# Kernel optimization log

Measured on AMD Instinct MI355X. Metric: run time of the kernel, lower is better.

The kernel has to match this reference:

```python
import jax, jax.numpy as jnp
import numpy as np

B, N, E = 64, 256, 512   # batch, leaves (power of 2), embed_size
D, U = 512, 512          # tree_size, units (controller size == units)


def setup_inputs() -> dict:
    key = jax.random.key(0)
    ks = jax.random.split(key, 11)
    sc = lambda k, shape: jax.random.normal(k, shape, dtype=jnp.float32) * 0.05
    return {
        "inputs": jax.random.normal(ks[0], (B, N, E), dtype=jnp.float32),
        "h0": sc(ks[1], (B, U)),
        "c0": sc(ks[2], (B, U)),
        "W_t": sc(ks[3], (E, D)),          # Transformer
        "W_j": sc(ks[4], (2 * D, D)),      # Join
        "W_s": sc(ks[5], (D + U, 1)),      # Search
        "W_h": sc(ks[6], (D + U, D)),      # Write candidate
        "W_T": sc(ks[7], (D + U, 1)),      # Write gate
        "kernel": sc(ks[8], (E, 4 * U)),   # LSTM input kernel (i,f,c,o)
        "rec_kernel": sc(ks[9], (U, 4 * U)),
        "bias": jnp.zeros((4 * U,), jnp.float32),
    }


def reference(inputs, h0, c0, W_t, W_j, W_s, W_h, W_T, kernel, rec_kernel, bias):
    b, n, e = inputs.shape
    control = h0  # control = previous LSTM hidden state

    # --- leaf embed: Transformer, batched over all leaves ---
    leaf_h = jax.nn.relu(jnp.einsum('bne,ed->bnd', inputs, W_t))  # [B,N,D]

    # --- refresh: bottom-up join, batched per tree level ---
    levels = [leaf_h]
    h = leaf_h
    while h.shape[1] > 1:
        pair = jnp.concatenate([h[:, 0::2], h[:, 1::2]], axis=-1)  # [B,m/2,2D]
        h = jax.nn.relu(jnp.einsum('bmk,kd->bmd', pair, W_j))
        levels.append(h)

    # --- retrieve: top-down search producing leaf attentions ---
    # Searches all use refresh-time h (parent search happens before any
    # update in its subtree), so a level-batched top-down pass is exact.
    attn = jnp.ones((b, 1, 1), inputs.dtype)
    for lvl in range(len(levels) - 1, 0, -1):
        node_h = levels[lvl]                     # [B,m,D]
        m = node_h.shape[1]
        ctrl = jnp.broadcast_to(control[:, None, :], (b, m, control.shape[-1]))
        mr = jax.nn.sigmoid(jnp.einsum('bmk,ko->bmo',
                                       jnp.concatenate([node_h, ctrl], -1), W_s))  # [B,m,1]
        # children interleave: left gets attn*(1-mr), right gets attn*mr
        attn = jnp.concatenate([attn * (1.0 - mr), attn * mr], axis=-1).reshape(b, 2 * m, 1)

    tree_out = jnp.sum(attn * inputs, axis=1)  # [B,E] soft-retrieved leaf value

    # --- write update of leaf memories, batched over all leaves ---
    ctrl = jnp.broadcast_to(control[:, None, :], (b, n, control.shape[-1]))
    data = jnp.concatenate([leaf_h, ctrl], -1)                     # [B,N,D+U]
    cand = jax.nn.sigmoid(jnp.einsum('bnk,kd->bnd', data, W_h))
    upd = jax.nn.sigmoid(jnp.einsum('bnk,ko->bno', data, W_T))
    written = upd * cand + (1.0 - upd) * leaf_h
    leaf_h_new = attn * written + (1.0 - attn) * leaf_h            # [B,N,D]

    # --- LSTM cell update (keras LSTMCell gate order i,f,c,o) ---
    z = tree_out @ kernel + h0 @ rec_kernel + bias
    zi, zf, zg, zo = jnp.split(z, 4, axis=-1)
    c_new = jax.nn.sigmoid(zf) * c0 + jax.nn.sigmoid(zi) * jnp.tanh(zg)
    h_new = jax.nn.sigmoid(zo) * jnp.tanh(c_new)
    return h_new, c_new, leaf_h_new
```

## Files before the change

### kernel.cpp

```cpp
#include <hip/hip_runtime.h>
#include <hip/hip_bf16.h>
#include <cstdint>
#include <cstddef>


__device__ __forceinline__ float sigmoidf_(float x) { return 1.0f / (1.0f + __expf(-x)); }

typedef __attribute__((ext_vector_type(8))) short bf16x8;
typedef __attribute__((ext_vector_type(4))) float f32x4;

__device__ __forceinline__ void load_lds16(const void* g, void* l) {
  __builtin_amdgcn_global_load_lds((const __attribute__((address_space(1))) void*)g,
                                   (__attribute__((address_space(3))) void*)l, 16, 0, 0);
}

__global__ __launch_bounds__(256)
void cvt_inputs(const float* __restrict__ in, __hip_bfloat16* __restrict__ outp) {
  const size_t i = ((size_t)blockIdx.x * 256 + threadIdx.x) * 8;
  float4 v0 = *(const float4*)(in + i);
  float4 v1 = *(const float4*)(in + i + 4);
  union { __hip_bfloat16 h[8]; bf16x8 v; } u;
  u.h[0] = __float2bfloat16(v0.x); u.h[1] = __float2bfloat16(v0.y);
  u.h[2] = __float2bfloat16(v0.z); u.h[3] = __float2bfloat16(v0.w);
  u.h[4] = __float2bfloat16(v1.x); u.h[5] = __float2bfloat16(v1.y);
  u.h[6] = __float2bfloat16(v1.z); u.h[7] = __float2bfloat16(v1.w);
  *(bf16x8*)(outp + i) = u.v;
}

__global__ __launch_bounds__(256)
void tconv_all(const float* __restrict__ W_t, const float* __restrict__ W_j,
               const float* __restrict__ W_h,
               __hip_bfloat16* __restrict__ Wt_t, __hip_bfloat16* __restrict__ Wt_j,
               __hip_bfloat16* __restrict__ Wt_h) {
  const int z = blockIdx.z;
  if (z != 1 && blockIdx.x >= 16) return;
  const int K = (z == 1) ? 1024 : 512;
  const float* W = (z == 0) ? W_t : ((z == 1) ? W_j : W_h);
  __hip_bfloat16* Wt = (z == 0) ? Wt_t : ((z == 1) ? Wt_j : Wt_h);
  __shared__ float sh[32][33];
  const int tx = threadIdx.x & 31, ty = threadIdx.x >> 5;
  const int k0 = blockIdx.x * 32, n0 = blockIdx.y * 32;
#pragma unroll
  for (int i = 0; i < 4; ++i)
    sh[ty + i * 8][tx] = W[(size_t)(k0 + ty + i * 8) * 512 + n0 + tx];
  __syncthreads();
#pragma unroll
  for (int i = 0; i < 4; ++i)
    Wt[(size_t)(n0 + ty + i * 8) * K + k0 + tx] = __float2bfloat16(sh[tx][ty + i * 8]);
}

template<int MODE, bool AFP32>
__global__ __launch_bounds__(256)
void mfma_gemm(const __hip_bfloat16* __restrict__ A, const float* __restrict__ Af,
               const __hip_bfloat16* __restrict__ Bt, int M, int K,
               __hip_bfloat16* __restrict__ Cb, float* __restrict__ Cf,
               const float* __restrict__ ctrl_h, const float* __restrict__ attn,
               const float* __restrict__ upd, const __hip_bfloat16* __restrict__ leaf) {
  __shared__ __align__(16) __hip_bfloat16 Asm[2][128 * 32];
  __shared__ __align__(16) __hip_bfloat16 Bsm[2][128 * 32];
  const int tid = threadIdx.x;
  const int wave = tid >> 6, lane = tid & 63;
  const int bm = blockIdx.x * 128, bn = blockIdx.y * 128;
  const int wm = (wave >> 1) * 64, wn = (wave & 1) * 64;
  const int q = lane >> 4, lr = lane & 15;

  f32x4 acc[4][4] = {};

  const int c0 = wave * 128 + lane, c1 = c0 + 64;
  const size_t ga0 = (size_t)(bm + (c0 >> 2)) * K + (c0 & 3) * 8;
  const size_t ga1 = (size_t)(bm + (c1 >> 2)) * K + (c1 & 3) * 8;
  const size_t gb0 = (size_t)(bn + (c0 >> 2)) * K + (c0 & 3) * 8;
  const size_t gb1 = (size_t)(bn + (c1 >> 2)) * K + (c1 & 3) * 8;

  if constexpr (AFP32) {
    for (int k0v = 0; k0v < K; k0v += 32) {
#pragma unroll
      for (int it = 0; it < 4; ++it) {
        const int c = it * 256 + tid;
        const int row = c >> 3, kc = c & 7;
        float4 v = *(const float4*)(Af + (size_t)(bm + row) * K + k0v + kc * 4);
        __hip_bfloat16 h[4] = {__float2bfloat16(v.x), __float2bfloat16(v.y),
                               __float2bfloat16(v.z), __float2bfloat16(v.w)};
        *(ushort4*)(Asm[0] + row * 32 + kc * 4) = *(ushort4*)h;
      }
      load_lds16(Bt + gb0 + k0v, Bsm[0] + wave * 1024);
      load_lds16(Bt + gb1 + k0v, Bsm[0] + wave * 1024 + 512);
      __syncthreads();
      bf16x8 af[4], bfr[4];
#pragma unroll
      for (int mt = 0; mt < 4; ++mt)
        af[mt] = *(const bf16x8*)(Asm[0] + (wm + mt * 16 + lr) * 32 + q * 8);
#pragma unroll
      for (int nt = 0; nt < 4; ++nt)
        bfr[nt] = *(const bf16x8*)(Bsm[0] + (wn + nt * 16 + lr) * 32 + q * 8);
#pragma unroll
      for (int mt = 0; mt < 4; ++mt)
#pragma unroll
        for (int nt = 0; nt < 4; ++nt)
          acc[mt][nt] = __builtin_amdgcn_mfma_f32_16x16x32_bf16(af[mt], bfr[nt], acc[mt][nt], 0, 0, 0);
      __syncthreads();
    }
  } else {
    auto stage = [&](int s, int kv) {
      load_lds16(A + ga0 + kv, Asm[s] + wave * 1024);
      load_lds16(A + ga1 + kv, Asm[s] + wave * 1024 + 512);
      load_lds16(Bt + gb0 + kv, Bsm[s] + wave * 1024);
      load_lds16(Bt + gb1 + kv, Bsm[s] + wave * 1024 + 512);
    };
    stage(0, 0);
    __syncthreads();
    int cur = 0;
    for (int kv = 0; kv < K; kv += 32) {
      if (kv + 32 < K) stage(cur ^ 1, kv + 32);
      bf16x8 af[4], bfr[4];
#pragma unroll
      for (int mt = 0; mt < 4; ++mt)
        af[mt] = *(const bf16x8*)(Asm[cur] + (wm + mt * 16 + lr) * 32 + q * 8);
#pragma unroll
      for (int nt = 0; nt < 4; ++nt)
        bfr[nt] = *(const bf16x8*)(Bsm[cur] + (wn + nt * 16 + lr) * 32 + q * 8);
#pragma unroll
      for (int mt = 0; mt < 4; ++mt)
#pragma unroll
        for (int nt = 0; nt < 4; ++nt)
          acc[mt][nt] = __builtin_amdgcn_mfma_f32_16x16x32_bf16(af[mt], bfr[nt], acc[mt][nt], 0, 0, 0);
      __syncthreads();
      cur ^= 1;
    }
  }

  if (MODE == 0) {
#pragma unroll
    for (int mt = 0; mt < 4; ++mt) {
      const int rbase = bm + wm + mt * 16 + q * 4;
#pragma unroll
      for (int nt = 0; nt < 4; ++nt) {
        const int col = bn + wn + nt * 16 + lr;
#pragma unroll
        for (int r = 0; r < 4; ++r) {
          const int row = rbase + r;
          if (row < M)
            Cb[(size_t)row * 512 + col] = __float2bfloat16(fmaxf(acc[mt][nt][r], 0.f));
        }
      }
    }
  } else {
#pragma unroll
    for (int mt = 0; mt < 4; ++mt) {
      const int rbase = bm + wm + mt * 16 + q * 4;
#pragma unroll
      for (int r = 0; r < 4; ++r) {
        const int row = rbase + r;
        const float a = attn[row];
        const float u = upd[row];
        const int bidx = row >> 8;
#pragma unroll
        for (int nt = 0; nt < 4; ++nt) {
          const int col = bn + wn + nt * 16 + lr;
          const float cand = sigmoidf_(acc[mt][nt][r] + ctrl_h[(size_t)bidx * 512 + col]);
          const float lf = __bfloat162float(leaf[(size_t)row * 512 + col]);
          const float w = u * cand + (1.f - u) * lf;
          Cf[(size_t)row * 512 + col] = a * w + (1.f - a) * lf;
        }
      }
    }
  }
}

__global__ __launch_bounds__(256)
void join_level(const __hip_bfloat16* __restrict__ in, __hip_bfloat16* __restrict__ outp,
                const __hip_bfloat16* __restrict__ Wt_j) {
  const int wave = threadIdx.x >> 6, lane = threadIdx.x & 63;
  const int q = lane >> 4, lr = lane & 15;
  const int tile = blockIdx.x * 4 + wave;
  const int mtile = tile >> 5, ntile = tile & 31;
  const __hip_bfloat16* ap = in + (size_t)(mtile * 16 + lr) * 1024 + q * 8;
  const __hip_bfloat16* bp = Wt_j + (size_t)(ntile * 16 + lr) * 1024 + q * 8;
  f32x4 acc = {0.f, 0.f, 0.f, 0.f};
#pragma unroll 8
  for (int k0 = 0; k0 < 1024; k0 += 32) {
    bf16x8 a  = *(const bf16x8*)(ap + k0);
    bf16x8 bb = *(const bf16x8*)(bp + k0);
    acc = __builtin_amdgcn_mfma_f32_16x16x32_bf16(a, bb, acc, 0, 0, 0);
  }
  const int col = ntile * 16 + lr;
  const int orow = mtile * 16 + q * 4;
#pragma unroll
  for (int r = 0; r < 4; ++r)
    outp[(size_t)(orow + r) * 512 + col] = __float2bfloat16(fmaxf(acc[r], 0.f));
}

__global__ __launch_bounds__(256)
void gemv_upd(const __hip_bfloat16* __restrict__ leaf, const float* __restrict__ W_T,
              const float* __restrict__ ctrlT, float* __restrict__ upd) {
  const int wave = threadIdx.x >> 6, lane = threadIdx.x & 63;
  const int row = blockIdx.x * 4 + wave;
  union { bf16x8 v; __hip_bfloat16 e[8]; } u;
  u.v = *(const bf16x8*)(leaf + (size_t)row * 512 + lane * 8);
  const float* wp = W_T + lane * 8;
  float p = 0.f;
#pragma unroll
  for (int j = 0; j < 8; ++j) p += __bfloat162float(u.e[j]) * wp[j];
#pragma unroll
  for (int off = 32; off > 0; off >>= 1) p += __shfl_down(p, off);
  if (lane == 0) upd[row] = sigmoidf_(p + ctrlT[row >> 8]);
}

__global__ __launch_bounds__(256)
void ctrl_prep(const float* __restrict__ h0, const float* __restrict__ W_h,
               const float* __restrict__ W_T, float* __restrict__ ch,
               float* __restrict__ ctrlT) {
  const int b = blockIdx.y, tid = threadIdx.x;
  if (blockIdx.x == 2) {
    __shared__ float part[256];
    float p = 0.f;
    for (int i = tid; i < 512; i += 256) p += h0[b * 512 + i] * W_T[512 + i];
    part[tid] = p; __syncthreads();
    for (int s = 128; s > 0; s >>= 1) { if (tid < s) part[tid] += part[tid + s]; __syncthreads(); }
    if (tid == 0) ctrlT[b] = part[0];
  } else {
    __shared__ float hsh[512];
    hsh[tid]       = h0[b * 512 + tid];
    hsh[tid + 256] = h0[b * 512 + 256 + tid];
    __syncthreads();
    const int col = blockIdx.x * 256 + tid;
    const float* Wp = W_h + (size_t)512 * 512 + col;
    float s = 0.f;
#pragma unroll 8
    for (int k = 0; k < 512; ++k) s += hsh[k] * Wp[(size_t)k * 512];
    ch[(size_t)b * 512 + col] = s;
  }
}

__global__ __launch_bounds__(256)
void propagate_sc(const __hip_bfloat16* __restrict__ levels, const float* __restrict__ h0,
                  const float* __restrict__ W_s, float* __restrict__ attn_out) {
  const int b = blockIdx.x, tid = threadIdx.x;
  const int wave = tid >> 6, lane = tid & 63;
  __shared__ float part[256], ws[512], sc_sh[256], attn_sh[256], newattn[256];
  __shared__ float scs_sh;
  ws[tid] = W_s[tid]; ws[tid + 256] = W_s[tid + 256];
  float p = 0.f;
  for (int i = tid; i < 512; i += 256) p += h0[b * 512 + i] * W_s[512 + i];
  part[tid] = p; __syncthreads();
  for (int s = 128; s > 0; s >>= 1) { if (tid < s) part[tid] += part[tid + s]; __syncthreads(); }
  if (tid == 0) { scs_sh = part[0]; attn_sh[0] = 1.f; }
  __syncthreads();
  const float scs = scs_sh;
  const int rowbase[9] = {0, 0, 8192, 12288, 14336, 15360, 15872, 16128, 16256};
  const int nodeoff[9] = {0, 0, 128, 192, 224, 240, 248, 252, 254};
  for (int l = 1; l <= 8; ++l) {
    const int m = 256 >> l;
    for (int j0 = wave * 8; j0 < m; j0 += 32) {
      const int j = j0 + (lane >> 3), s = lane & 7;
      float q = 0.f;
      if (j < m) {
        const __hip_bfloat16* xr = levels + (size_t)(rowbase[l] + b * m + j) * 512;
#pragma unroll
        for (int i = 0; i < 8; ++i) {
          const int k = (i * 8 + s) * 8;
          union { bf16x8 v; __hip_bfloat16 e[8]; } u;
          u.v = *(const bf16x8*)(xr + k);
#pragma unroll
          for (int jj = 0; jj < 8; ++jj) q += __bfloat162float(u.e[jj]) * ws[k + jj];
        }
      }
      q += __shfl_xor(q, 1); q += __shfl_xor(q, 2); q += __shfl_xor(q, 4);
      if (s == 0 && j < m) sc_sh[nodeoff[l] + j] = q;
    }
  }
  __syncthreads();
#pragma unroll
  for (int l = 8; l >= 1; --l) {
    const int m = 256 >> l;
    if (tid < m) {
      const float mr = sigmoidf_(sc_sh[nodeoff[l] + tid] + scs);
      const float a = attn_sh[tid];
      newattn[2 * tid]     = a * (1.f - mr);
      newattn[2 * tid + 1] = a * mr;
    }
    __syncthreads();
    if (tid < 2 * m) attn_sh[tid] = newattn[tid];
    __syncthreads();
  }
  attn_out[b * 256 + tid] = attn_sh[tid];
}

__global__ __launch_bounds__(256)
void tree_part(const float* __restrict__ inputs, const float* __restrict__ attn,
               float* __restrict__ tp) {
  const int s = blockIdx.x, b = blockIdx.y;
  const int tid = threadIdx.x;
  __shared__ float a_sh[64];
  if (tid < 64) a_sh[tid] = attn[b * 256 + s * 64 + tid];
  __syncthreads();
  float acc0 = 0.f, acc1 = 0.f;
  const float* base = inputs + ((size_t)b * 256 + s * 64) * 512;
  for (int nn = 0; nn < 64; ++nn) {
    const float a = a_sh[nn];
    const float* row = base + (size_t)nn * 512;
    acc0 += a * row[tid];
    acc1 += a * row[tid + 256];
  }
  tp[((size_t)s * 64 + b) * 512 + tid]       = acc0;
  tp[((size_t)s * 64 + b) * 512 + tid + 256] = acc1;
}

__global__ __launch_bounds__(256)
void lstm_fused(const float* __restrict__ tp, const float* __restrict__ h0,
                const float* __restrict__ kern, const float* __restrict__ rec,
                const float* __restrict__ bias, const float* __restrict__ c0,
                float* __restrict__ out_h, float* __restrict__ out_c) {
  const int tid = threadIdx.x;
  const int ug = tid & 63, gate = tid >> 6;
  const int b0 = blockIdx.y * 4;
  __shared__ float xs[4][512], hs[4][512];
  for (int i = tid; i < 2048; i += 256) {
    const int bb = i >> 9, k = i & 511;
    const size_t idx = (size_t)(b0 + bb) * 512 + k;
    xs[bb][k] = tp[idx] + tp[32768 + idx] + tp[65536 + idx] + tp[98304 + idx];
    hs[bb][k] = h0[idx];
  }
  __syncthreads();
  const int col = gate * 512 + blockIdx.x * 64 + ug;
  float a0 = bias[col], a1 = a0, a2 = a0, a3 = a0;
#pragma unroll 4
  for (int k = 0; k < 512; ++k) {
    const float wk = kern[(size_t)k * 2048 + col];
    const float wr = rec[(size_t)k * 2048 + col];
    a0 += xs[0][k] * wk + hs[0][k] * wr;
    a1 += xs[1][k] * wk + hs[1][k] * wr;
    a2 += xs[2][k] * wk + hs[2][k] * wr;
    a3 += xs[3][k] * wk + hs[3][k] * wr;
  }
  __shared__ float zs[4][4][64];
  zs[gate][0][ug] = a0; zs[gate][1][ug] = a1;
  zs[gate][2][ug] = a2; zs[gate][3][ug] = a3;
  __syncthreads();
  const int cb = tid >> 6, cu = tid & 63;
  const float zi = zs[0][cb][cu], zf = zs[1][cb][cu];
  const float zg = zs[2][cb][cu], zo = zs[3][cb][cu];
  const int gi = (b0 + cb) * 512 + blockIdx.x * 64 + cu;
  const float c = sigmoidf_(zf) * c0[gi] + sigmoidf_(zi) * tanhf(zg);
  out_h[gi] = sigmoidf_(zo) * tanhf(c);
  out_c[gi] = c;
}

extern "C" void kernel_launch(void* const* d_in, const int* in_sizes, int n_in,
                              void* d_out, int out_size, void* d_ws, size_t ws_size,
                              hipStream_t stream) {
  const float* inputs = (const float*)d_in[0];
  const float* h0     = (const float*)d_in[1];
  const float* c0     = (const float*)d_in[2];
  const float* W_t    = (const float*)d_in[3];
  const float* W_j    = (const float*)d_in[4];
  const float* W_s    = (const float*)d_in[5];
  const float* W_h    = (const float*)d_in[6];
  const float* W_T    = (const float*)d_in[7];
  const float* kern   = (const float*)d_in[8];
  const float* rec    = (const float*)d_in[9];
  const float* bias   = (const float*)d_in[10];
  float* out = (float*)d_out;

  char* p = (char*)d_ws;
  __hip_bfloat16* leaf_bf   = (__hip_bfloat16*)p; p += 16777216;
  __hip_bfloat16* levels_bf = (__hip_bfloat16*)p; p += 16842752;
  __hip_bfloat16* Wt_t      = (__hip_bfloat16*)p; p += 524288;
  __hip_bfloat16* Wt_j      = (__hip_bfloat16*)p; p += 1048576;
  __hip_bfloat16* Wt_h      = (__hip_bfloat16*)p; p += 524288;
  float* attn  = (float*)p; p += 65536;
  float* upd   = (float*)p; p += 65536;
  float* ch    = (float*)p; p += 131072;
  float* ctrlT = (float*)p; p += 4096;
  float* tp    = (float*)p; p += 524288;
  const bool use_cvt = ws_size >= (size_t)(p - (char*)d_ws) + 16777216;
  __hip_bfloat16* inputs_bf = (__hip_bfloat16*)p;

  tconv_all<<<dim3(32, 16, 3), 256, 0, stream>>>(W_t, W_j, W_h, Wt_t, Wt_j, Wt_h);
  ctrl_prep<<<dim3(3, 64), 256, 0, stream>>>(h0, W_h, W_T, ch, ctrlT);

  if (use_cvt) {
    cvt_inputs<<<4096, 256, 0, stream>>>(inputs, inputs_bf);
    mfma_gemm<0, false><<<dim3(128, 4), 256, 0, stream>>>(
        inputs_bf, nullptr, Wt_t, 16384, 512,
        leaf_bf, nullptr, nullptr, nullptr, nullptr, nullptr);
  } else {
    mfma_gemm<0, true><<<dim3(128, 4), 256, 0, stream>>>(
        nullptr, inputs, Wt_t, 16384, 512,
        leaf_bf, nullptr, nullptr, nullptr, nullptr, nullptr);
  }

  const int lvl_off_h[9] = {0, 0, 4194304, 6291456, 7340032,
                            7864320, 8126464, 8257536, 8323072};
  const __hip_bfloat16* Aptr = leaf_bf;
  for (int l = 1; l <= 3; ++l) {
    const int M = 64 * (256 >> l);
    __hip_bfloat16* Cl = levels_bf + lvl_off_h[l];
    mfma_gemm<0, false><<<dim3(M / 128, 4), 256, 0, stream>>>(
        Aptr, nullptr, Wt_j, M, 1024,
        Cl, nullptr, nullptr, nullptr, nullptr, nullptr);
    Aptr = Cl;
  }
  for (int l = 4; l <= 8; ++l) {
    const int m_out = 256 >> l;
    join_level<<<32 * m_out, 256, 0, stream>>>(levels_bf + lvl_off_h[l - 1],
                                               levels_bf + lvl_off_h[l], Wt_j);
  }

  gemv_upd<<<4096, 256, 0, stream>>>(leaf_bf, W_T, ctrlT, upd);
  propagate_sc<<<64, 256, 0, stream>>>(levels_bf, h0, W_s, attn);

  tree_part<<<dim3(4, 64), 256, 0, stream>>>(inputs, attn, tp);

  mfma_gemm<1, false><<<dim3(128, 4), 256, 0, stream>>>(
      leaf_bf, nullptr, Wt_h, 16384, 512,
      nullptr, out + 65536, ch, attn, upd, leaf_bf);

  lstm_fused<<<dim3(8, 16), 256, 0, stream>>>(tp, h0, kern, rec, bias, c0, out, out + 32768);
}
```

Measured before the change: 389.7 us.

## Fuse upd gemv into leaf GEMM epilogue and split-K the LSTM gate GEMM

```diff
diff --git a/kernel.cpp b/kernel.cpp
--- a/kernel.cpp
+++ b/kernel.cpp
@@ -55,7 +55,8 @@
                const __hip_bfloat16* __restrict__ Bt, int M, int K,
                __hip_bfloat16* __restrict__ Cb, float* __restrict__ Cf,
                const float* __restrict__ ctrl_h, const float* __restrict__ attn,
-               const float* __restrict__ upd, const __hip_bfloat16* __restrict__ leaf) {
+               const float* __restrict__ upd_raw, const __hip_bfloat16* __restrict__ leaf,
+               const float* __restrict__ W_T, const float* __restrict__ ctrlT) {
   __shared__ __align__(16) __hip_bfloat16 Asm[2][128 * 32];
   __shared__ __align__(16) __hip_bfloat16 Bsm[2][128 * 32];
   const int tid = threadIdx.x;
@@ -144,6 +145,27 @@
         }
       }
     }
+    if (upd_raw) {
+      float wt[4];
+#pragma unroll
+      for (int nt = 0; nt < 4; ++nt) wt[nt] = W_T[bn + wn + nt * 16 + lr];
+#pragma unroll
+      for (int mt = 0; mt < 4; ++mt) {
+        const int rbase = bm + wm + mt * 16 + q * 4;
+#pragma unroll
+        for (int r = 0; r < 4; ++r) {
+          float p = 0.f;
+#pragma unroll
+          for (int nt = 0; nt < 4; ++nt) {
+            const float v = __bfloat162float(__float2bfloat16(fmaxf(acc[mt][nt][r], 0.f)));
+            p += v * wt[nt];
+          }
+          p += __shfl_xor(p, 1); p += __shfl_xor(p, 2);
+          p += __shfl_xor(p, 4); p += __shfl_xor(p, 8);
+          if (lr == 0) atomicAdd((float*)&upd_raw[rbase + r], p);
+        }
+      }
+    }
   } else {
 #pragma unroll
     for (int mt = 0; mt < 4; ++mt) {
@@ -152,8 +174,8 @@
       for (int r = 0; r < 4; ++r) {
         const int row = rbase + r;
         const float a = attn[row];
-        const float u = upd[row];
         const int bidx = row >> 8;
+        const float u = sigmoidf_(upd_raw[row] + ctrlT[bidx]);
 #pragma unroll
         for (int nt = 0; nt < 4; ++nt) {
           const int col = bn + wn + nt * 16 + lr;
@@ -188,22 +210,6 @@
 #pragma unroll
   for (int r = 0; r < 4; ++r)
     outp[(size_t)(orow + r) * 512 + col] = __float2bfloat16(fmaxf(acc[r], 0.f));
-}
-
-__global__ __launch_bounds__(256)
-void gemv_upd(const __hip_bfloat16* __restrict__ leaf, const float* __restrict__ W_T,
-              const float* __restrict__ ctrlT, float* __restrict__ upd) {
-  const int wave = threadIdx.x >> 6, lane = threadIdx.x & 63;
-  const int row = blockIdx.x * 4 + wave;
-  union { bf16x8 v; __hip_bfloat16 e[8]; } u;
-  u.v = *(const bf16x8*)(leaf + (size_t)row * 512 + lane * 8);
-  const float* wp = W_T + lane * 8;
-  float p = 0.f;
-#pragma unroll
-  for (int j = 0; j < 8; ++j) p += __bfloat162float(u.e[j]) * wp[j];
-#pragma unroll
-  for (int off = 32; off > 0; off >>= 1) p += __shfl_down(p, off);
-  if (lane == 0) upd[row] = sigmoidf_(p + ctrlT[row >> 8]);
 }
 
 __global__ __launch_bounds__(256)
@@ -307,43 +313,59 @@
 }
 
 __global__ __launch_bounds__(256)
-void lstm_fused(const float* __restrict__ tp, const float* __restrict__ h0,
-                const float* __restrict__ kern, const float* __restrict__ rec,
-                const float* __restrict__ bias, const float* __restrict__ c0,
-                float* __restrict__ out_h, float* __restrict__ out_c) {
+void lstm_gemm_splitk(const float* __restrict__ tp, const float* __restrict__ h0,
+                      const float* __restrict__ kern, const float* __restrict__ rec,
+                      float* __restrict__ Zp) {
   const int tid = threadIdx.x;
-  const int ug = tid & 63, gate = tid >> 6;
+  const int col = blockIdx.x * 256 + tid;
   const int b0 = blockIdx.y * 4;
-  __shared__ float xs[4][512], hs[4][512];
-  for (int i = tid; i < 2048; i += 256) {
-    const int bb = i >> 9, k = i & 511;
-    const size_t idx = (size_t)(b0 + bb) * 512 + k;
-    xs[bb][k] = tp[idx] + tp[32768 + idx] + tp[65536 + idx] + tp[98304 + idx];
-    hs[bb][k] = h0[idx];
+  const int z = blockIdx.z;
+  const float* W = (z < 4) ? (kern + (size_t)z * 128 * 2048)
+                           : (rec + (size_t)(z - 4) * 128 * 2048);
+  const int koff = (z & 3) * 128;
+  __shared__ float xs[4][128];
+  for (int i = tid; i < 512; i += 256) {
+    int bb = i >> 7, k = i & 127;
+    const size_t idx = (size_t)(b0 + bb) * 512 + koff + k;
+    float x;
+    if (z < 4) x = tp[idx] + tp[32768 + idx] + tp[65536 + idx] + tp[98304 + idx];
+    else       x = h0[idx];
+    xs[bb][k] = x;
   }
   __syncthreads();
-  const int col = gate * 512 + blockIdx.x * 64 + ug;
-  float a0 = bias[col], a1 = a0, a2 = a0, a3 = a0;
-#pragma unroll 4
-  for (int k = 0; k < 512; ++k) {
-    const float wk = kern[(size_t)k * 2048 + col];
-    const float wr = rec[(size_t)k * 2048 + col];
-    a0 += xs[0][k] * wk + hs[0][k] * wr;
-    a1 += xs[1][k] * wk + hs[1][k] * wr;
-    a2 += xs[2][k] * wk + hs[2][k] * wr;
-    a3 += xs[3][k] * wk + hs[3][k] * wr;
-  }
-  __shared__ float zs[4][4][64];
-  zs[gate][0][ug] = a0; zs[gate][1][ug] = a1;
-  zs[gate][2][ug] = a2; zs[gate][3][ug] = a3;
-  __syncthreads();
-  const int cb = tid >> 6, cu = tid & 63;
-  const float zi = zs[0][cb][cu], zf = zs[1][cb][cu];
-  const float zg = zs[2][cb][cu], zo = zs[3][cb][cu];
-  const int gi = (b0 + cb) * 512 + blockIdx.x * 64 + cu;
-  const float c = sigmoidf_(zf) * c0[gi] + sigmoidf_(zi) * tanhf(zg);
-  out_h[gi] = sigmoidf_(zo) * tanhf(c);
-  out_c[gi] = c;
+  float a0 = 0.f, a1 = 0.f, a2 = 0.f, a3 = 0.f;
+#pragma unroll 8
+  for (int k = 0; k < 128; ++k) {
+    const float w = W[(size_t)k * 2048 + col];
+    a0 += xs[0][k] * w;
+    a1 += xs[1][k] * w;
+    a2 += xs[2][k] * w;
+    a3 += xs[3][k] * w;
+  }
+  Zp[((size_t)z * 64 + b0 + 0) * 2048 + col] = a0;
+  Zp[((size_t)z * 64 + b0 + 1) * 2048 + col] = a1;
+  Zp[((size_t)z * 64 + b0 + 2) * 2048 + col] = a2;
+  Zp[((size_t)z * 64 + b0 + 3) * 2048 + col] = a3;
+}
+
+__global__ __launch_bounds__(256)
+void lstm_combine(const float* __restrict__ Zp, const float* __restrict__ bias,
+                  const float* __restrict__ c0,
+                  float* __restrict__ out_h, float* __restrict__ out_c) {
+  const int i = blockIdx.x * 256 + threadIdx.x;
+  const int b = i >> 9, u = i & 511;
+  float zi = bias[u], zf = bias[512 + u], zg = bias[1024 + u], zo = bias[1536 + u];
+#pragma unroll
+  for (int z = 0; z < 8; ++z) {
+    const size_t base = ((size_t)z * 64 + b) * 2048;
+    zi += Zp[base + u];
+    zf += Zp[base + 512 + u];
+    zg += Zp[base + 1024 + u];
+    zo += Zp[base + 1536 + u];
+  }
+  const float c = sigmoidf_(zf) * c0[i] + sigmoidf_(zi) * tanhf(zg);
+  out_h[i] = sigmoidf_(zo) * tanhf(c);
+  out_c[i] = c;
 }
 
 extern "C" void kernel_launch(void* const* d_in, const int* in_sizes, int n_in,
@@ -373,21 +395,23 @@
   float* ch    = (float*)p; p += 131072;
   float* ctrlT = (float*)p; p += 4096;
   float* tp    = (float*)p; p += 524288;
+  float* Zp    = (float*)p; p += 4194304;
   const bool use_cvt = ws_size >= (size_t)(p - (char*)d_ws) + 16777216;
   __hip_bfloat16* inputs_bf = (__hip_bfloat16*)p;
 
   tconv_all<<<dim3(32, 16, 3), 256, 0, stream>>>(W_t, W_j, W_h, Wt_t, Wt_j, Wt_h);
   ctrl_prep<<<dim3(3, 64), 256, 0, stream>>>(h0, W_h, W_T, ch, ctrlT);
+  hipMemsetAsync(upd, 0, 16384 * sizeof(float), stream);
 
   if (use_cvt) {
     cvt_inputs<<<4096, 256, 0, stream>>>(inputs, inputs_bf);
     mfma_gemm<0, false><<<dim3(128, 4), 256, 0, stream>>>(
         inputs_bf, nullptr, Wt_t, 16384, 512,
-        leaf_bf, nullptr, nullptr, nullptr, nullptr, nullptr);
+        leaf_bf, nullptr, nullptr, nullptr, upd, nullptr, W_T, nullptr);
   } else {
     mfma_gemm<0, true><<<dim3(128, 4), 256, 0, stream>>>(
         nullptr, inputs, Wt_t, 16384, 512,
-        leaf_bf, nullptr, nullptr, nullptr, nullptr, nullptr);
+        leaf_bf, nullptr, nullptr, nullptr, upd, nullptr, W_T, nullptr);
   }
 
   const int lvl_off_h[9] = {0, 0, 4194304, 6291456, 7340032,
@@ -398,7 +422,7 @@
     __hip_bfloat16* Cl = levels_bf + lvl_off_h[l];
     mfma_gemm<0, false><<<dim3(M / 128, 4), 256, 0, stream>>>(
         Aptr, nullptr, Wt_j, M, 1024,
-        Cl, nullptr, nullptr, nullptr, nullptr, nullptr);
+        Cl, nullptr, nullptr, nullptr, nullptr, nullptr, nullptr, nullptr);
     Aptr = Cl;
   }
   for (int l = 4; l <= 8; ++l) {
@@ -407,14 +431,14 @@
                                                levels_bf + lvl_off_h[l], Wt_j);
   }
 
-  gemv_upd<<<4096, 256, 0, stream>>>(leaf_bf, W_T, ctrlT, upd);
   propagate_sc<<<64, 256, 0, stream>>>(levels_bf, h0, W_s, attn);
 
   tree_part<<<dim3(4, 64), 256, 0, stream>>>(inputs, attn, tp);
 
   mfma_gemm<1, false><<<dim3(128, 4), 256, 0, stream>>>(
       leaf_bf, nullptr, Wt_h, 16384, 512,
-      nullptr, out + 65536, ch, attn, upd, leaf_bf);
-
-  lstm_fused<<<dim3(8, 16), 256, 0, stream>>>(tp, h0, kern, rec, bias, c0, out, out + 32768);
-}
+      nullptr, out + 65536, ch, attn, upd, leaf_bf, nullptr, ctrlT);
+
+  lstm_gemm_splitk<<<dim3(8, 16, 8), 256, 0, stream>>>(tp, h0, kern, rec, Zp);
+  lstm_combine<<<128, 256, 0, stream>>>(Zp, bias, c0, out, out + 32768);
+}
```

New measurement: 334.4 us. -14.2%, faster.
